# Performance work log

Measured on AMD Instinct MI355X. Metric: run time of the kernel, lower is better.

The kernel has to match this reference:

```python
import jax, jax.numpy as jnp
import numpy as np


def setup_inputs() -> dict:
    key = jax.random.key(0)
    ks = jax.random.split(key, 11)
    b, c, h, w = 16, 64, 16, 16
    F = 64  # num_filters
    O = 64  # num_outputs
    d_in = 2 * (c + 1)  # 130: concat of two (feature + coord) vectors
    s = 0.05
    return {
        "x_img": jax.random.normal(ks[0], (b, c, h, w), dtype=jnp.float32),
        "Wg0": jax.random.normal(ks[1], (F, d_in), dtype=jnp.float32) * s,
        "bg0": jax.random.normal(ks[2], (F,), dtype=jnp.float32) * s,
        "Wg1": jax.random.normal(ks[3], (F, F), dtype=jnp.float32) * s,
        "bg1": jax.random.normal(ks[4], (F,), dtype=jnp.float32) * s,
        "Wg2": jax.random.normal(ks[5], (F, F), dtype=jnp.float32) * s,
        "bg2": jax.random.normal(ks[6], (F,), dtype=jnp.float32) * s,
        "Wp": jax.random.normal(ks[7], (F, F), dtype=jnp.float32) * s,
        "bp": jax.random.normal(ks[8], (F,), dtype=jnp.float32) * s,
        "Wo": jax.random.normal(ks[9], (O, F), dtype=jnp.float32) * s,
        "bo": jax.random.normal(ks[10], (O,), dtype=jnp.float32) * s,
    }


def reference(x_img, Wg0, bg0, Wg1, bg1, Wg2, bg2, Wp, bp, Wo, bo):
    b, c, h, w = x_img.shape
    L = h * w
    # [b, L, c]: flatten spatial, move channels last
    feats = x_img.reshape(b, c, L).transpose(0, 2, 1)
    # append 1-d coordinate feature -> [b, L, c+1]
    coord = jnp.broadcast_to(
        jnp.arange(L, dtype=feats.dtype).reshape(1, L, 1), (b, L, 1)
    )
    feats = jnp.concatenate([feats, coord], axis=2)
    # pairwise broadcast-concat: pair[b, p, q] = [feats[b, q], feats[b, p]]
    d = feats.shape[-1]
    x_i = jnp.broadcast_to(feats[:, None, :, :], (b, L, L, d))
    x_j = jnp.broadcast_to(feats[:, :, None, :], (b, L, L, d))
    pair = jnp.concatenate([x_i, x_j], axis=3)  # [b, L, L, 2*(c+1)]
    # shared g-MLP (3 layers, ReLU)
    out = jax.nn.relu(jnp.einsum("bpqd,fd->bpqf", pair, Wg0) + bg0)
    out = jax.nn.relu(jnp.einsum("bpqf,gf->bpqg", out, Wg1) + bg1)
    out = jax.nn.relu(jnp.einsum("bpqf,gf->bpqg", out, Wg2) + bg2)
    # sum-reduce over both pair dims -> [b, F]
    out = out.sum(axis=(1, 2))
    # f-network
    out = jax.nn.relu(out @ Wp.T + bp)
    out = out @ Wo.T + bo
    return out
```

## Files before the change

### kernel.cpp

```cpp
#include <hip/hip_runtime.h>


typedef short s8v __attribute__((ext_vector_type(8)));
typedef short s4v __attribute__((ext_vector_type(4)));
typedef float f4v __attribute__((ext_vector_type(4)));
typedef unsigned u4v __attribute__((ext_vector_type(4)));
typedef unsigned u2v __attribute__((ext_vector_type(2)));

#define KEEP(x) asm volatile("" : "+v"(x))

#define MFMA16(a, b, c) __builtin_amdgcn_mfma_f32_16x16x16bf16_1k(a, b, c, 0, 0, 0)

__device__ __forceinline__ unsigned pkrh(float a, float b) {
  unsigned ua = __builtin_bit_cast(unsigned, a) + 0x8000u;
  unsigned ub = __builtin_bit_cast(unsigned, b) + 0x8000u;
  return (ua >> 16) | (ub & 0xFFFF0000u);
}
__device__ __forceinline__ f4v relu4(f4v v) {
  f4v z = {0.f, 0.f, 0.f, 0.f};
  return __builtin_elementwise_max(v, z);
}
__device__ __forceinline__ s8v cvt8(f4v a, f4v b) {
  u4v u = {pkrh(a[0], a[1]), pkrh(a[2], a[3]),
           pkrh(b[0], b[1]), pkrh(b[2], b[3])};
  return __builtin_bit_cast(s8v, u);
}
__device__ __forceinline__ s4v cvt4(f4v a) {
  u2v u = {pkrh(a[0], a[1]), pkrh(a[2], a[3])};
  return __builtin_bit_cast(s4v, u);
}
__device__ __forceinline__ f4v ldf4(const float* p) {
  return *(const f4v*)p;
}

__global__ __launch_bounds__(256) void k_pre(
    const float* __restrict__ x, const float* __restrict__ Wg0,
    const float* __restrict__ bg0, float* __restrict__ Ag,
    float* __restrict__ Bg) {
  __shared__ float ws[64 * 131];
  __shared__ float xs[64 * 17];

  const int t = threadIdx.x;
  const int b = blockIdx.x >> 4;
  const int l0 = (blockIdx.x & 15) * 16;

  for (int i = t; i < 64 * 130; i += 256) {
    int f = i / 130, d = i - f * 130;
    ws[f * 131 + d] = Wg0[i];
  }
  for (int i = t; i < 64 * 16; i += 256) {
    int ch = i >> 4, li = i & 15;
    xs[ch * 17 + li] = x[b * 16384 + ch * 256 + l0 + li];
  }
  __syncthreads();

  const int f = t & 63;
  const int w = t >> 6;
  float accA[4] = {0.f, 0.f, 0.f, 0.f};
  float accB[4] = {0.f, 0.f, 0.f, 0.f};
  for (int d = 0; d < 64; ++d) {
    float wa = ws[f * 131 + d];
    float wb = ws[f * 131 + 65 + d];
#pragma unroll
    for (int i = 0; i < 4; ++i) {
      float xv = xs[d * 17 + w + 4 * i];
      accA[i] += xv * wa;
      accB[i] += xv * wb;
    }
  }
  const float wca = ws[f * 131 + 64];
  const float wcb = ws[f * 131 + 129];
  const float bias = bg0[f];
#pragma unroll
  for (int i = 0; i < 4; ++i) {
    int l = l0 + w + 4 * i;
    Ag[(b * 256 + l) * 64 + f] = accA[i] + (float)l * wca;
    Bg[(b * 256 + l) * 64 + f] = accB[i] + (float)l * wcb + bias;
  }
}

__global__ __launch_bounds__(256, 3) void k_main(
    const float* __restrict__ Ag, const float* __restrict__ Bg,
    const float* __restrict__ Wg1, const float* __restrict__ bg1,
    const float* __restrict__ Wg2, const float* __restrict__ bg2,
    float* __restrict__ Part) {
  __shared__ __align__(16) float Bs[16 * 64];
  __shared__ float Sblk[64];

  const int t = threadIdx.x;
  const int wid = t >> 6;
  const int lane = t & 63;
  const int mm = lane & 15;
  const int quad = lane >> 4;
  const int b = blockIdx.y;
  const int blkx = blockIdx.x;
  const int qq = blkx & 3;
  const int p0 = (blkx >> 2) * 16;
  const int q0 = (qq * 4 + wid) * 16;

  if (t < 64) Sblk[t] = 0.f;

  {
    const f4v* Bb4 = (const f4v*)(Bg + (b * 256 + p0) * 64);
    ((f4v*)Bs)[t] = Bb4[t];
  }

  const float* Arow = Ag + (b * 256 + q0 + mm) * 64;
  f4v af0 = ldf4(Arow + quad * 8);
  f4v af1 = ldf4(Arow + quad * 8 + 4);
  f4v af2 = ldf4(Arow + 32 + quad * 8);
  f4v af3 = ldf4(Arow + 36 + quad * 8);

  s8v W1f[4][2];
  s4v W2f[4][4];
  f4v c1i[4], c2i[4];
#pragma unroll
  for (int gt = 0; gt < 4; ++gt) {
    c1i[gt] = ldf4(bg1 + gt * 16 + quad * 4);
    c2i[gt] = ldf4(bg2 + gt * 16 + quad * 4);
#pragma unroll
    for (int kh = 0; kh < 2; ++kh) {
      const float* r1 = Wg1 + (gt * 16 + mm) * 64 + kh * 32 + quad * 8;
      W1f[gt][kh] = cvt8(ldf4(r1), ldf4(r1 + 4));
    }
#pragma unroll
    for (int kt = 0; kt < 4; ++kt) {
      const float* r2 = Wg2 + (gt * 16 + mm) * 64 + kt * 16 + quad * 4;
      W2f[gt][kt] = cvt4(ldf4(r2));
    }
  }
#pragma unroll
  for (int gt = 0; gt < 4; ++gt) {
    KEEP(W1f[gt][0]); KEEP(W1f[gt][1]);
    KEEP(W2f[gt][0]); KEEP(W2f[gt][1]); KEEP(W2f[gt][2]); KEEP(W2f[gt][3]);
    KEEP(c1i[gt]); KEEP(c2i[gt]);
  }
  KEEP(af0); KEEP(af1); KEEP(af2); KEEP(af3);

  __syncthreads();

  f4v cs[4] = {{0.f,0.f,0.f,0.f},{0.f,0.f,0.f,0.f},
               {0.f,0.f,0.f,0.f},{0.f,0.f,0.f,0.f}};

#pragma unroll 4
  for (int ip = 0; ip < 16; ++ip) {
    const float* brow = Bs + ip * 64;
    f4v bq0 = ldf4(brow + quad * 8);
    f4v bq1 = ldf4(brow + quad * 8 + 4);
    f4v bq2 = ldf4(brow + 32 + quad * 8);
    f4v bq3 = ldf4(brow + 36 + quad * 8);

    s8v x0 = cvt8(relu4(af0 + bq0), relu4(af1 + bq1));
    s8v x1 = cvt8(relu4(af2 + bq2), relu4(af3 + bq3));

    s4v pk[4];
#pragma unroll
    for (int gt = 0; gt < 4; ++gt) {
      f4v a = c1i[gt];
      a = __builtin_amdgcn_mfma_f32_16x16x32_bf16(W1f[gt][0], x0, a, 0, 0, 0);
      a = __builtin_amdgcn_mfma_f32_16x16x32_bf16(W1f[gt][1], x1, a, 0, 0, 0);
      pk[gt] = cvt4(relu4(a));
    }
#pragma unroll
    for (int ot = 0; ot < 4; ++ot) {
      f4v a = c2i[ot];
      a = MFMA16(W2f[ot][0], pk[0], a);
      a = MFMA16(W2f[ot][1], pk[1], a);
      a = MFMA16(W2f[ot][2], pk[2], a);
      a = MFMA16(W2f[ot][3], pk[3], a);
      cs[ot] += relu4(a);
    }
  }

#pragma unroll
  for (int ot = 0; ot < 4; ++ot) {
#pragma unroll
    for (int r = 0; r < 4; ++r) {
      float v = cs[ot][r];
      v += __shfl_xor(v, 1);
      v += __shfl_xor(v, 2);
      v += __shfl_xor(v, 4);
      v += __shfl_xor(v, 8);
      if (mm == 0) atomicAdd(&Sblk[ot * 16 + quad * 4 + r], v);
    }
  }
  __syncthreads();
  if (t < 64) Part[(b * 64 + blkx) * 64 + t] = Sblk[t];
}

__global__ __launch_bounds__(64) void k_final(
    const float* __restrict__ Part, const float* __restrict__ Wp,
    const float* __restrict__ bp, const float* __restrict__ Wo,
    const float* __restrict__ bo, float* __restrict__ out) {
  __shared__ float sv[64], tv[64];
  const int b = blockIdx.x, t = threadIdx.x;
  float s = 0.f;
  const float* Pb = Part + b * 64 * 64;
#pragma unroll
  for (int j = 0; j < 64; ++j) s += Pb[j * 64 + t];
  sv[t] = s;
  __syncthreads();
  float acc = bp[t];
  for (int g = 0; g < 64; ++g) acc += sv[g] * Wp[t * 64 + g];
  tv[t] = fmaxf(acc, 0.f);
  __syncthreads();
  float o = bo[t];
  for (int f = 0; f < 64; ++f) o += tv[f] * Wo[t * 64 + f];
  out[b * 64 + t] = o;
}

extern "C" void kernel_launch(void* const* d_in, const int* in_sizes, int n_in,
                              void* d_out, int out_size, void* d_ws, size_t ws_size,
                              hipStream_t stream) {
  const float* x   = (const float*)d_in[0];
  const float* Wg0 = (const float*)d_in[1];
  const float* bg0 = (const float*)d_in[2];
  const float* Wg1 = (const float*)d_in[3];
  const float* bg1 = (const float*)d_in[4];
  const float* Wg2 = (const float*)d_in[5];
  const float* bg2 = (const float*)d_in[6];
  const float* Wp  = (const float*)d_in[7];
  const float* bp  = (const float*)d_in[8];
  const float* Wo  = (const float*)d_in[9];
  const float* bo  = (const float*)d_in[10];
  float* out = (float*)d_out;

  float* Ag   = (float*)d_ws;
  float* Bg   = Ag + 16 * 256 * 64;
  float* Part = Bg + 16 * 256 * 64;

  k_pre<<<256, 256, 0, stream>>>(x, Wg0, bg0, Ag, Bg);
  k_main<<<dim3(64, 16), 256, 0, stream>>>(Ag, Bg, Wg1, bg1, Wg2, bg2, Part);
  k_final<<<16, 64, 0, stream>>>(Part, Wp, bp, Wo, bo, out);
}
```

Baseline: 128.6 us.

## Process two B rows per iteration with interleaved MFMA chains, halve grid

Each k_main block now covers 32 p-rows instead of 16, halving the grid to 512 blocks and the partial-sum count fed to k_final. The inner loop handles two p-rows at once and interleaves two independent MFMA accumulation chains, to hide MFMA dependency latency within a wave. The LDS atomicAdd reduction is replaced by per-wave slots summed by the first 64 threads. Launch bounds drop from 3 to 1 blocks per CU, which raises the register budget but may lower occupancy. The smaller grid of 512 blocks on a 256-CU device can also leave CUs unevenly loaded.

Result: faster. 120.3 us (-6.5%).

```diff
diff --git a/kernel.cpp b/kernel.cpp
--- a/kernel.cpp
+++ b/kernel.cpp
@@ -9,6 +9,7 @@
 
 #define KEEP(x) asm volatile("" : "+v"(x))
 
+#define MFMA32(a, b, c) __builtin_amdgcn_mfma_f32_16x16x32_bf16(a, b, c, 0, 0, 0)
 #define MFMA16(a, b, c) __builtin_amdgcn_mfma_f32_16x16x16bf16_1k(a, b, c, 0, 0, 0)
 
 __device__ __forceinline__ unsigned pkrh(float a, float b) {
@@ -79,13 +80,13 @@
   }
 }
 
-__global__ __launch_bounds__(256, 3) void k_main(
+__global__ __launch_bounds__(256, 1) void k_main(
     const float* __restrict__ Ag, const float* __restrict__ Bg,
     const float* __restrict__ Wg1, const float* __restrict__ bg1,
     const float* __restrict__ Wg2, const float* __restrict__ bg2,
     float* __restrict__ Part) {
-  __shared__ __align__(16) float Bs[16 * 64];
-  __shared__ float Sblk[64];
+  __shared__ __align__(16) float Bs[32 * 64];
+  __shared__ float Sw[4][64];
 
   const int t = threadIdx.x;
   const int wid = t >> 6;
@@ -95,14 +96,13 @@
   const int b = blockIdx.y;
   const int blkx = blockIdx.x;
   const int qq = blkx & 3;
-  const int p0 = (blkx >> 2) * 16;
+  const int p0 = (blkx >> 2) * 32;
   const int q0 = (qq * 4 + wid) * 16;
-
-  if (t < 64) Sblk[t] = 0.f;
 
   {
     const f4v* Bb4 = (const f4v*)(Bg + (b * 256 + p0) * 64);
     ((f4v*)Bs)[t] = Bb4[t];
+    ((f4v*)Bs)[t + 256] = Bb4[t + 256];
   }
 
   const float* Arow = Ag + (b * 256 + q0 + mm) * 64;
@@ -142,33 +142,49 @@
   f4v cs[4] = {{0.f,0.f,0.f,0.f},{0.f,0.f,0.f,0.f},
                {0.f,0.f,0.f,0.f},{0.f,0.f,0.f,0.f}};
 
-#pragma unroll 4
-  for (int ip = 0; ip < 16; ++ip) {
-    const float* brow = Bs + ip * 64;
-    f4v bq0 = ldf4(brow + quad * 8);
-    f4v bq1 = ldf4(brow + quad * 8 + 4);
-    f4v bq2 = ldf4(brow + 32 + quad * 8);
-    f4v bq3 = ldf4(brow + 36 + quad * 8);
-
-    s8v x0 = cvt8(relu4(af0 + bq0), relu4(af1 + bq1));
-    s8v x1 = cvt8(relu4(af2 + bq2), relu4(af3 + bq3));
-
-    s4v pk[4];
+#pragma unroll 2
+  for (int ip = 0; ip < 32; ip += 2) {
+    const float* brA = Bs + ip * 64;
+    const float* brB = brA + 64;
+    f4v a0 = ldf4(brA + quad * 8);
+    f4v a1 = ldf4(brA + quad * 8 + 4);
+    f4v a2 = ldf4(brA + 32 + quad * 8);
+    f4v a3 = ldf4(brA + 36 + quad * 8);
+    f4v b0 = ldf4(brB + quad * 8);
+    f4v b1 = ldf4(brB + quad * 8 + 4);
+    f4v b2 = ldf4(brB + 32 + quad * 8);
+    f4v b3 = ldf4(brB + 36 + quad * 8);
+
+    s8v xA0 = cvt8(relu4(af0 + a0), relu4(af1 + a1));
+    s8v xA1 = cvt8(relu4(af2 + a2), relu4(af3 + a3));
+    s8v xB0 = cvt8(relu4(af0 + b0), relu4(af1 + b1));
+    s8v xB1 = cvt8(relu4(af2 + b2), relu4(af3 + b3));
+
+    s4v pkA[4], pkB[4];
 #pragma unroll
     for (int gt = 0; gt < 4; ++gt) {
-      f4v a = c1i[gt];
-      a = __builtin_amdgcn_mfma_f32_16x16x32_bf16(W1f[gt][0], x0, a, 0, 0, 0);
-      a = __builtin_amdgcn_mfma_f32_16x16x32_bf16(W1f[gt][1], x1, a, 0, 0, 0);
-      pk[gt] = cvt4(relu4(a));
+      f4v uA = c1i[gt];
+      f4v uB = c1i[gt];
+      uA = MFMA32(W1f[gt][0], xA0, uA);
+      uB = MFMA32(W1f[gt][0], xB0, uB);
+      uA = MFMA32(W1f[gt][1], xA1, uA);
+      uB = MFMA32(W1f[gt][1], xB1, uB);
+      pkA[gt] = cvt4(relu4(uA));
+      pkB[gt] = cvt4(relu4(uB));
     }
 #pragma unroll
     for (int ot = 0; ot < 4; ++ot) {
-      f4v a = c2i[ot];
-      a = MFMA16(W2f[ot][0], pk[0], a);
-      a = MFMA16(W2f[ot][1], pk[1], a);
-      a = MFMA16(W2f[ot][2], pk[2], a);
-      a = MFMA16(W2f[ot][3], pk[3], a);
-      cs[ot] += relu4(a);
+      f4v uA = c2i[ot];
+      f4v uB = c2i[ot];
+      uA = MFMA16(W2f[ot][0], pkA[0], uA);
+      uB = MFMA16(W2f[ot][0], pkB[0], uB);
+      uA = MFMA16(W2f[ot][1], pkA[1], uA);
+      uB = MFMA16(W2f[ot][1], pkB[1], uB);
+      uA = MFMA16(W2f[ot][2], pkA[2], uA);
+      uB = MFMA16(W2f[ot][2], pkB[2], uB);
+      uA = MFMA16(W2f[ot][3], pkA[3], uA);
+      uB = MFMA16(W2f[ot][3], pkB[3], uB);
+      cs[ot] += relu4(uA) + relu4(uB);
     }
   }
 
@@ -181,11 +197,13 @@
       v += __shfl_xor(v, 2);
       v += __shfl_xor(v, 4);
       v += __shfl_xor(v, 8);
-      if (mm == 0) atomicAdd(&Sblk[ot * 16 + quad * 4 + r], v);
-    }
-  }
-  __syncthreads();
-  if (t < 64) Part[(b * 64 + blkx) * 64 + t] = Sblk[t];
+      if (mm == 0) Sw[wid][ot * 16 + quad * 4 + r] = v;
+    }
+  }
+  __syncthreads();
+  if (t < 64)
+    Part[(b * 32 + blkx) * 64 + t] =
+        Sw[0][t] + Sw[1][t] + Sw[2][t] + Sw[3][t];
 }
 
 __global__ __launch_bounds__(64) void k_final(
@@ -195,9 +213,9 @@
   __shared__ float sv[64], tv[64];
   const int b = blockIdx.x, t = threadIdx.x;
   float s = 0.f;
-  const float* Pb = Part + b * 64 * 64;
-#pragma unroll
-  for (int j = 0; j < 64; ++j) s += Pb[j * 64 + t];
+  const float* Pb = Part + b * 32 * 64;
+#pragma unroll
+  for (int j = 0; j < 32; ++j) s += Pb[j * 64 + t];
   sv[t] = s;
   __syncthreads();
   float acc = bp[t];
@@ -230,6 +248,6 @@
   float* Part = Bg + 16 * 256 * 64;
 
   k_pre<<<256, 256, 0, stream>>>(x, Wg0, bg0, Ag, Bg);
-  k_main<<<dim3(64, 16), 256, 0, stream>>>(Ag, Bg, Wg1, bg1, Wg2, bg2, Part);
+  k_main<<<dim3(32, 16), 256, 0, stream>>>(Ag, Bg, Wg1, bg1, Wg2, bg2, Part);
   k_final<<<16, 64, 0, stream>>>(Part, Wp, bp, Wo, bo, out);
 }
```

## Switch main pairwise MLP to 32x32x16 bf16 MFMA tiles with lane-swap repacking

Applied to the files above, without the earlier changes.

Rewrites the main kernel so each wavefront processes 32 q-positions using 32x32x16 bf16 MFMAs instead of 16x16 tiles. Layer-1 outputs are converted to bf16 and exchanged across half-wavefronts with shuffles to form the layer-2 B operand. Biases are now added after the MFMA (packed as bf16) rather than used as accumulator init. The grid is halved to 32 blocks per batch and launch bounds drop to one block per SIMD. The aim is fewer, larger MFMA instructions and less per-tile overhead, at the cost of more registers, extra shuffles, and bias values rounded to bf16.

Result: slower. 131.9 us (+2.6%).

```diff
diff --git a/kernel.cpp b/kernel.cpp
--- a/kernel.cpp
+++ b/kernel.cpp
@@ -2,20 +2,25 @@
 
 
 typedef short s8v __attribute__((ext_vector_type(8)));
-typedef short s4v __attribute__((ext_vector_type(4)));
 typedef float f4v __attribute__((ext_vector_type(4)));
+typedef float f16v __attribute__((ext_vector_type(16)));
 typedef unsigned u4v __attribute__((ext_vector_type(4)));
-typedef unsigned u2v __attribute__((ext_vector_type(2)));
 
 #define KEEP(x) asm volatile("" : "+v"(x))
 
-#define MFMA16(a, b, c) __builtin_amdgcn_mfma_f32_16x16x16bf16_1k(a, b, c, 0, 0, 0)
+#define MFMA3216(a, b, c) __builtin_amdgcn_mfma_f32_32x32x16_bf16(a, b, c, 0, 0, 0)
 
 __device__ __forceinline__ unsigned pkrh(float a, float b) {
   unsigned ua = __builtin_bit_cast(unsigned, a) + 0x8000u;
   unsigned ub = __builtin_bit_cast(unsigned, b) + 0x8000u;
   return (ua >> 16) | (ub & 0xFFFF0000u);
 }
+__device__ __forceinline__ float lo16f(unsigned w) {
+  return __builtin_bit_cast(float, w << 16);
+}
+__device__ __forceinline__ float hi16f(unsigned w) {
+  return __builtin_bit_cast(float, w & 0xFFFF0000u);
+}
 __device__ __forceinline__ f4v relu4(f4v v) {
   f4v z = {0.f, 0.f, 0.f, 0.f};
   return __builtin_elementwise_max(v, z);
@@ -25,12 +30,12 @@
            pkrh(b[0], b[1]), pkrh(b[2], b[3])};
   return __builtin_bit_cast(s8v, u);
 }
-__device__ __forceinline__ s4v cvt4(f4v a) {
-  u2v u = {pkrh(a[0], a[1]), pkrh(a[2], a[3])};
-  return __builtin_bit_cast(s4v, u);
-}
 __device__ __forceinline__ f4v ldf4(const float* p) {
   return *(const f4v*)p;
+}
+__device__ __forceinline__ f16v zero16() {
+  f16v v = {0.f,0.f,0.f,0.f,0.f,0.f,0.f,0.f,0.f,0.f,0.f,0.f,0.f,0.f,0.f,0.f};
+  return v;
 }
 
 __global__ __launch_bounds__(256) void k_pre(
@@ -79,113 +84,171 @@
   }
 }
 
-__global__ __launch_bounds__(256, 3) void k_main(
+__global__ __launch_bounds__(256, 1) void k_main(
     const float* __restrict__ Ag, const float* __restrict__ Bg,
     const float* __restrict__ Wg1, const float* __restrict__ bg1,
     const float* __restrict__ Wg2, const float* __restrict__ bg2,
     float* __restrict__ Part) {
   __shared__ __align__(16) float Bs[16 * 64];
-  __shared__ float Sblk[64];
+  __shared__ float Sw[4][64];
 
   const int t = threadIdx.x;
   const int wid = t >> 6;
   const int lane = t & 63;
-  const int mm = lane & 15;
-  const int quad = lane >> 4;
+  const int n = lane & 31;
+  const int h = lane >> 5;
   const int b = blockIdx.y;
   const int blkx = blockIdx.x;
-  const int qq = blkx & 3;
-  const int p0 = (blkx >> 2) * 16;
-  const int q0 = (qq * 4 + wid) * 16;
-
-  if (t < 64) Sblk[t] = 0.f;
+  const int qh = blkx & 1;
+  const int p0 = (blkx >> 1) * 16;
+  const int q = qh * 128 + wid * 32 + n;
 
   {
     const f4v* Bb4 = (const f4v*)(Bg + (b * 256 + p0) * 64);
     ((f4v*)Bs)[t] = Bb4[t];
   }
 
-  const float* Arow = Ag + (b * 256 + q0 + mm) * 64;
-  f4v af0 = ldf4(Arow + quad * 8);
-  f4v af1 = ldf4(Arow + quad * 8 + 4);
-  f4v af2 = ldf4(Arow + 32 + quad * 8);
-  f4v af3 = ldf4(Arow + 36 + quad * 8);
-
-  s8v W1f[4][2];
-  s4v W2f[4][4];
-  f4v c1i[4], c2i[4];
-#pragma unroll
-  for (int gt = 0; gt < 4; ++gt) {
-    c1i[gt] = ldf4(bg1 + gt * 16 + quad * 4);
-    c2i[gt] = ldf4(bg2 + gt * 16 + quad * 4);
-#pragma unroll
-    for (int kh = 0; kh < 2; ++kh) {
-      const float* r1 = Wg1 + (gt * 16 + mm) * 64 + kh * 32 + quad * 8;
-      W1f[gt][kh] = cvt8(ldf4(r1), ldf4(r1 + 4));
-    }
-#pragma unroll
-    for (int kt = 0; kt < 4; ++kt) {
-      const float* r2 = Wg2 + (gt * 16 + mm) * 64 + kt * 16 + quad * 4;
-      W2f[gt][kt] = cvt4(ldf4(r2));
-    }
-  }
-#pragma unroll
-  for (int gt = 0; gt < 4; ++gt) {
-    KEEP(W1f[gt][0]); KEEP(W1f[gt][1]);
-    KEEP(W2f[gt][0]); KEEP(W2f[gt][1]); KEEP(W2f[gt][2]); KEEP(W2f[gt][3]);
-    KEEP(c1i[gt]); KEEP(c2i[gt]);
-  }
-  KEEP(af0); KEEP(af1); KEEP(af2); KEEP(af3);
-
-  __syncthreads();
-
-  f4v cs[4] = {{0.f,0.f,0.f,0.f},{0.f,0.f,0.f,0.f},
-               {0.f,0.f,0.f,0.f},{0.f,0.f,0.f,0.f}};
-
-#pragma unroll 4
+  const float* Arow = Ag + (b * 256 + q) * 64 + h * 8;
+  f4v af[4][2];
+#pragma unroll
+  for (int seg = 0; seg < 4; ++seg) {
+    af[seg][0] = ldf4(Arow + seg * 16);
+    af[seg][1] = ldf4(Arow + seg * 16 + 4);
+  }
+
+  s8v W1A[2][4], W2A[2][4];
+#pragma unroll
+  for (int mt = 0; mt < 2; ++mt) {
+#pragma unroll
+    for (int seg = 0; seg < 4; ++seg) {
+      const float* r1 = Wg1 + (mt * 32 + n) * 64 + seg * 16 + h * 8;
+      const float* r2 = Wg2 + (mt * 32 + n) * 64 + seg * 16 + h * 8;
+      W1A[mt][seg] = cvt8(ldf4(r1), ldf4(r1 + 4));
+      W2A[mt][seg] = cvt8(ldf4(r2), ldf4(r2 + 4));
+    }
+  }
+
+  u4v b1pv[2][2], b2pv[2][2];
+#pragma unroll
+  for (int mt = 0; mt < 2; ++mt) {
+    const float* s1 = bg1 + mt * 32 + 4 * h;
+    const float* s2 = bg2 + mt * 32 + 4 * h;
+    f4v v0 = ldf4(s1), v1 = ldf4(s1 + 8), v2 = ldf4(s1 + 16), v3 = ldf4(s1 + 24);
+    b1pv[mt][0] = (u4v){pkrh(v0[0], v0[1]), pkrh(v0[2], v0[3]),
+                        pkrh(v1[0], v1[1]), pkrh(v1[2], v1[3])};
+    b1pv[mt][1] = (u4v){pkrh(v2[0], v2[1]), pkrh(v2[2], v2[3]),
+                        pkrh(v3[0], v3[1]), pkrh(v3[2], v3[3])};
+    f4v u0 = ldf4(s2), u1 = ldf4(s2 + 8), u2 = ldf4(s2 + 16), u3 = ldf4(s2 + 24);
+    b2pv[mt][0] = (u4v){pkrh(u0[0], u0[1]), pkrh(u0[2], u0[3]),
+                        pkrh(u1[0], u1[1]), pkrh(u1[2], u1[3])};
+    b2pv[mt][1] = (u4v){pkrh(u2[0], u2[1]), pkrh(u2[2], u2[3]),
+                        pkrh(u3[0], u3[1]), pkrh(u3[2], u3[3])};
+  }
+
+#pragma unroll
+  for (int mt = 0; mt < 2; ++mt) {
+    KEEP(W1A[mt][0]); KEEP(W1A[mt][1]); KEEP(W1A[mt][2]); KEEP(W1A[mt][3]);
+    KEEP(W2A[mt][0]); KEEP(W2A[mt][1]); KEEP(W2A[mt][2]); KEEP(W2A[mt][3]);
+    KEEP(b1pv[mt][0]); KEEP(b1pv[mt][1]); KEEP(b2pv[mt][0]); KEEP(b2pv[mt][1]);
+  }
+#pragma unroll
+  for (int seg = 0; seg < 4; ++seg) { KEEP(af[seg][0]); KEEP(af[seg][1]); }
+
+  __syncthreads();
+
+  f16v cs[2] = {zero16(), zero16()};
+
+#pragma unroll 2
   for (int ip = 0; ip < 16; ++ip) {
-    const float* brow = Bs + ip * 64;
-    f4v bq0 = ldf4(brow + quad * 8);
-    f4v bq1 = ldf4(brow + quad * 8 + 4);
-    f4v bq2 = ldf4(brow + 32 + quad * 8);
-    f4v bq3 = ldf4(brow + 36 + quad * 8);
-
-    s8v x0 = cvt8(relu4(af0 + bq0), relu4(af1 + bq1));
-    s8v x1 = cvt8(relu4(af2 + bq2), relu4(af3 + bq3));
-
-    s4v pk[4];
-#pragma unroll
-    for (int gt = 0; gt < 4; ++gt) {
-      f4v a = c1i[gt];
-      a = __builtin_amdgcn_mfma_f32_16x16x32_bf16(W1f[gt][0], x0, a, 0, 0, 0);
-      a = __builtin_amdgcn_mfma_f32_16x16x32_bf16(W1f[gt][1], x1, a, 0, 0, 0);
-      pk[gt] = cvt4(relu4(a));
-    }
-#pragma unroll
-    for (int ot = 0; ot < 4; ++ot) {
-      f4v a = c2i[ot];
-      a = MFMA16(W2f[ot][0], pk[0], a);
-      a = MFMA16(W2f[ot][1], pk[1], a);
-      a = MFMA16(W2f[ot][2], pk[2], a);
-      a = MFMA16(W2f[ot][3], pk[3], a);
-      cs[ot] += relu4(a);
-    }
-  }
-
-#pragma unroll
-  for (int ot = 0; ot < 4; ++ot) {
-#pragma unroll
-    for (int r = 0; r < 4; ++r) {
-      float v = cs[ot][r];
-      v += __shfl_xor(v, 1);
-      v += __shfl_xor(v, 2);
-      v += __shfl_xor(v, 4);
-      v += __shfl_xor(v, 8);
-      if (mm == 0) atomicAdd(&Sblk[ot * 16 + quad * 4 + r], v);
-    }
-  }
-  __syncthreads();
-  if (t < 64) Part[(b * 64 + blkx) * 64 + t] = Sblk[t];
+    const float* br = Bs + ip * 64 + h * 8;
+    s8v xb[4];
+#pragma unroll
+    for (int seg = 0; seg < 4; ++seg) {
+      f4v b0 = ldf4(br + seg * 16);
+      f4v b1 = ldf4(br + seg * 16 + 4);
+      xb[seg] = cvt8(relu4(af[seg][0] + b0), relu4(af[seg][1] + b1));
+    }
+
+    unsigned pk[2][8];
+#pragma unroll
+    for (int mt = 0; mt < 2; ++mt) {
+      f16v u = zero16();
+      u = MFMA3216(W1A[mt][0], xb[0], u);
+      u = MFMA3216(W1A[mt][1], xb[1], u);
+      u = MFMA3216(W1A[mt][2], xb[2], u);
+      u = MFMA3216(W1A[mt][3], xb[3], u);
+#pragma unroll
+      for (int k = 0; k < 8; ++k) {
+        unsigned w = b1pv[mt][k >> 2][k & 3];
+        pk[mt][k] = pkrh(fmaxf(u[2 * k] + lo16f(w), 0.f),
+                         fmaxf(u[2 * k + 1] + hi16f(w), 0.f));
+      }
+    }
+
+    unsigned rcv[2][4];
+#pragma unroll
+    for (int mt = 0; mt < 2; ++mt) {
+      unsigned w0 = h ? pk[mt][0] : pk[mt][2];
+      unsigned w1 = h ? pk[mt][1] : pk[mt][3];
+      unsigned w2 = h ? pk[mt][4] : pk[mt][6];
+      unsigned w3 = h ? pk[mt][5] : pk[mt][7];
+      rcv[mt][0] = __shfl_xor(w0, 32);
+      rcv[mt][1] = __shfl_xor(w1, 32);
+      rcv[mt][2] = __shfl_xor(w2, 32);
+      rcv[mt][3] = __shfl_xor(w3, 32);
+    }
+
+    s8v y1b[4];
+#pragma unroll
+    for (int mt = 0; mt < 2; ++mt) {
+      u4v ya = (u4v){h ? rcv[mt][0] : pk[mt][0],
+                     h ? rcv[mt][1] : pk[mt][1],
+                     h ? pk[mt][2] : rcv[mt][0],
+                     h ? pk[mt][3] : rcv[mt][1]};
+      u4v yb = (u4v){h ? rcv[mt][2] : pk[mt][4],
+                     h ? rcv[mt][3] : pk[mt][5],
+                     h ? pk[mt][6] : rcv[mt][2],
+                     h ? pk[mt][7] : rcv[mt][3]};
+      y1b[mt * 2]     = __builtin_bit_cast(s8v, ya);
+      y1b[mt * 2 + 1] = __builtin_bit_cast(s8v, yb);
+    }
+
+#pragma unroll
+    for (int ot = 0; ot < 2; ++ot) {
+      f16v u = zero16();
+      u = MFMA3216(W2A[ot][0], y1b[0], u);
+      u = MFMA3216(W2A[ot][1], y1b[1], u);
+      u = MFMA3216(W2A[ot][2], y1b[2], u);
+      u = MFMA3216(W2A[ot][3], y1b[3], u);
+#pragma unroll
+      for (int k = 0; k < 16; ++k) {
+        unsigned w = b2pv[ot][(k >> 1) >> 2][(k >> 1) & 3];
+        float bb = (k & 1) ? hi16f(w) : lo16f(w);
+        cs[ot][k] += fmaxf(u[k] + bb, 0.f);
+      }
+    }
+  }
+
+#pragma unroll
+  for (int mt = 0; mt < 2; ++mt) {
+#pragma unroll
+    for (int m = 1; m < 32; m <<= 1) {
+#pragma unroll
+      for (int k = 0; k < 16; ++k)
+        cs[mt][k] += __shfl_xor(cs[mt][k], m);
+    }
+  }
+  if (n == 0) {
+#pragma unroll
+    for (int mt = 0; mt < 2; ++mt)
+#pragma unroll
+      for (int r = 0; r < 16; ++r)
+        Sw[wid][mt * 32 + (r & 3) + 8 * (r >> 2) + 4 * h] = cs[mt][r];
+  }
+  __syncthreads();
+  if (t < 64)
+    Part[(b * 32 + blkx) * 64 + t] =
+        Sw[0][t] + Sw[1][t] + Sw[2][t] + Sw[3][t];
 }
 
 __global__ __launch_bounds__(64) void k_final(
@@ -195,9 +258,9 @@
   __shared__ float sv[64], tv[64];
   const int b = blockIdx.x, t = threadIdx.x;
   float s = 0.f;
-  const float* Pb = Part + b * 64 * 64;
-#pragma unroll
-  for (int j = 0; j < 64; ++j) s += Pb[j * 64 + t];
+  const float* Pb = Part + b * 32 * 64;
+#pragma unroll
+  for (int j = 0; j < 32; ++j) s += Pb[j * 64 + t];
   sv[t] = s;
   __syncthreads();
   float acc = bp[t];
@@ -230,6 +293,6 @@
   float* Part = Bg + 16 * 256 * 64;
 
   k_pre<<<256, 256, 0, stream>>>(x, Wg0, bg0, Ag, Bg);
-  k_main<<<dim3(64, 16), 256, 0, stream>>>(Ag, Bg, Wg1, bg1, Wg2, bg2, Part);
+  k_main<<<dim3(32, 16), 256, 0, stream>>>(Ag, Bg, Wg1, bg1, Wg2, bg2, Part);
   k_final<<<16, 64, 0, stream>>>(Part, Wp, bp, Wo, bo, out);
 }
```
